# Performance work log

Hardware: AMD Instinct MI355X
Metric: run time of the kernel (lower is better)

## Reference

```python
import jax, jax.numpy as jnp
import numpy as np

NUM_HEADS = 16


def setup_inputs() -> dict:
    key = jax.random.key(0)
    ks = jax.random.split(key, 7)
    B_, N, C = 512, 64, 512
    x = jax.random.normal(ks[0], (B_, N, C), dtype=jnp.float32)
    attn_bias = jax.random.normal(ks[1], (NUM_HEADS, N, N), dtype=jnp.float32)
    mask = jax.random.normal(ks[2], (B_, N, N), dtype=jnp.float32)
    qkv_w = jax.random.normal(ks[3], (3 * C, C), dtype=jnp.float32) * (C ** -0.5)
    qkv_b = jax.random.normal(ks[4], (3 * C,), dtype=jnp.float32) * 0.02
    proj_w = jax.random.normal(ks[5], (C, C), dtype=jnp.float32) * (C ** -0.5)
    proj_b = jax.random.normal(ks[6], (C,), dtype=jnp.float32) * 0.02
    return {"x": x, "attn_bias": attn_bias, "mask": mask,
            "qkv_w": qkv_w, "qkv_b": qkv_b, "proj_w": proj_w, "proj_b": proj_b}


def reference(x, attn_bias, mask, qkv_w, qkv_b, proj_w, proj_b):
    B_, N, C = x.shape
    H = NUM_HEADS
    hd = C // H
    scale = hd ** -0.5
    # qkv projection: (B_, N, 3, H, hd) -> (3, B_, H, N, hd)
    qkv = (x @ qkv_w.T + qkv_b).reshape(B_, N, 3, H, hd)
    qkv = jnp.transpose(qkv, (2, 0, 3, 1, 4))
    q, k, v = qkv[0], qkv[1], qkv[2]
    attn = jnp.einsum('bhnd,bhmd->bhnm', q * scale, k)  # (B_, H, N, N)
    attn = attn + attn_bias            # (H, N, N) broadcasts over batch
    attn = attn + mask[:, None]        # (B_, 1, N, N)
    attn = jax.nn.softmax(attn, axis=-1)
    out = jnp.einsum('bhnm,bhmd->bhnd', attn, v)
    out = jnp.transpose(out, (0, 2, 1, 3)).reshape(B_, N, C)
    return out @ proj_w.T + proj_b
```

## Files before the change

### kernel.cpp

```cpp
#include <hip/hip_runtime.h>
#include <stdint.h>

typedef __attribute__((ext_vector_type(8))) __bf16 bf16x8;
typedef __attribute__((ext_vector_type(4))) float f32x4;
typedef __attribute__((ext_vector_type(4))) float fl4;
typedef __attribute__((ext_vector_type(8))) unsigned short us8;
typedef __attribute__((ext_vector_type(4))) unsigned short us4;

__device__ __forceinline__ unsigned short f2bf(float f) {
  union { float f; unsigned int u; } v;
  v.f = f;
  unsigned int r = v.u + 0x7FFFu + ((v.u >> 16) & 1u);
  return (unsigned short)(r >> 16);
}

#define GLOAD_LDS16(g, l)                                                   \
  __builtin_amdgcn_global_load_lds(                                         \
      (__attribute__((address_space(1))) void*)(g),                         \
      (__attribute__((address_space(3))) void*)(l), 16, 0, 0)

__global__ void f32_to_bf16_kernel(const float* __restrict__ in,
                                   unsigned short* __restrict__ out, int n) {
  int i = (blockIdx.x * blockDim.x + threadIdx.x) * 4;
  if (i + 3 < n) {
    fl4 v = *(const fl4*)(in + i);
    us4 o;
    o[0] = f2bf(v[0]);
    o[1] = f2bf(v[1]);
    o[2] = f2bf(v[2]);
    o[3] = f2bf(v[3]);
    *(us4*)(out + i) = o;
  }
}

template <bool OUT_BF16>
__global__ __launch_bounds__(256, 2) void gemm_nt_kernel(
    const unsigned short* __restrict__ A, const unsigned short* __restrict__ B,
    const float* __restrict__ bias, void* __restrict__ Cout, int M, int N,
    int K) {
  __shared__ __align__(16) unsigned short lA[128 * 64];
  __shared__ __align__(16) unsigned short lB[128 * 64];

  const int tid = threadIdx.x;
  const int lane = tid & 63;
  const int wid = tid >> 6;
  const int wr = (wid >> 1) * 64;
  const int wc = (wid & 1) * 64;
  const int bm = blockIdx.x * 128;
  const int bn = blockIdx.y * 128;

  const f32x4 zero4 = {0.f, 0.f, 0.f, 0.f};
  f32x4 acc[4][4];
#pragma unroll
  for (int m = 0; m < 4; ++m)
#pragma unroll
    for (int n = 0; n < 4; ++n) acc[m][n] = zero4;

  const int srow = tid >> 3;
  const int scol = (tid & 7) << 3;
  unsigned short* Ab = (unsigned short*)(A + (size_t)(bm + srow) * K + scol);
  unsigned short* Bb = (unsigned short*)(B + (size_t)(bn + srow) * K + scol);
  unsigned short* lAb = lA + srow * 64 + scol;
  unsigned short* lBb = lB + srow * 64 + scol;

  const int lr = lane & 15;
  const int lk8 = (lane >> 4) * 8;

  const int nkt = K >> 6;
  for (int kt = 0; kt < nkt; ++kt) {
#pragma unroll
    for (int i = 0; i < 4; ++i) {
      GLOAD_LDS16(Ab + (size_t)(i * 32) * K + kt * 64, lAb + i * 32 * 64);
      GLOAD_LDS16(Bb + (size_t)(i * 32) * K + kt * 64, lBb + i * 32 * 64);
    }
    asm volatile("s_waitcnt vmcnt(0)" ::: "memory");
    __syncthreads();
#pragma unroll
    for (int kk = 0; kk < 2; ++kk) {
      bf16x8 af[4], bfr[4];
#pragma unroll
      for (int m = 0; m < 4; ++m)
        af[m] = *(const bf16x8*)(lA + (wr + m * 16 + lr) * 64 + kk * 32 + lk8);
#pragma unroll
      for (int n = 0; n < 4; ++n)
        bfr[n] = *(const bf16x8*)(lB + (wc + n * 16 + lr) * 64 + kk * 32 + lk8);
#pragma unroll
      for (int m = 0; m < 4; ++m)
#pragma unroll
        for (int n = 0; n < 4; ++n)
          acc[m][n] = __builtin_amdgcn_mfma_f32_16x16x32_bf16(af[m], bfr[n],
                                                              acc[m][n], 0, 0, 0);
    }
    __syncthreads();
  }

  const int crow0 = bm + wr + (lane >> 4) * 4;
  const int ccol0 = bn + wc + lr;
#pragma unroll
  for (int n = 0; n < 4; ++n) {
    const int col = ccol0 + n * 16;
    const float bv = bias[col];
#pragma unroll
    for (int m = 0; m < 4; ++m) {
#pragma unroll
      for (int j = 0; j < 4; ++j) {
        const int row = crow0 + m * 16 + j;
        const float val = acc[m][n][j] + bv;
        if (OUT_BF16)
          ((unsigned short*)Cout)[(size_t)row * N + col] = f2bf(val);
        else
          ((float*)Cout)[(size_t)row * N + col] = val;
      }
    }
  }
}

__global__ __launch_bounds__(256, 2) void attn_kernel(
    const unsigned short* __restrict__ qkv, const float* __restrict__ abias,
    const float* __restrict__ mask, unsigned short* __restrict__ out) {
  __shared__ __align__(16) unsigned short lq[64 * 40];
  __shared__ __align__(16) unsigned short lk[64 * 40];
  __shared__ __align__(16) unsigned short lvT[32 * 72];
  __shared__ __align__(16) float ls[64 * 68];
  __shared__ __align__(16) unsigned short lp[64 * 72];

  const int blk = blockIdx.x;
  const int b = blk >> 4;
  const int h = blk & 15;
  const int tid = threadIdx.x;
  const int lane = tid & 63;
  const int wid = tid >> 6;
  const int lr = lane & 15;
  const int lk8 = (lane >> 4) * 8;

  {
    const int r = tid >> 2;
    const int d0 = (tid & 3) * 8;
    const size_t base = (size_t)(b * 64 + r) * 1536 + h * 32 + d0;
    us8 qv = *(const us8*)(qkv + base);
    us8 kv = *(const us8*)(qkv + base + 512);
    us8 vv = *(const us8*)(qkv + base + 1024);
    *(us8*)(lq + r * 40 + d0) = qv;
    *(us8*)(lk + r * 40 + d0) = kv;
#pragma unroll
    for (int i = 0; i < 8; ++i) lvT[(d0 + i) * 72 + r] = vv[i];
  }
  __syncthreads();

  f32x4 s[4];
  {
    bf16x8 aq = *(const bf16x8*)(lq + (wid * 16 + lr) * 40 + lk8);
#pragma unroll
    for (int n = 0; n < 4; ++n) {
      bf16x8 bk = *(const bf16x8*)(lk + (n * 16 + lr) * 40 + lk8);
      f32x4 z = {0.f, 0.f, 0.f, 0.f};
      s[n] = __builtin_amdgcn_mfma_f32_16x16x32_bf16(aq, bk, z, 0, 0, 0);
    }
  }
  const float scale = 0.17677669529663687f;
  const int sr0 = wid * 16 + (lane >> 4) * 4;
#pragma unroll
  for (int n = 0; n < 4; ++n) {
    const int col = n * 16 + lr;
#pragma unroll
    for (int j = 0; j < 4; ++j) {
      const int row = sr0 + j;
      ls[row * 68 + col] = s[n][j] * scale + abias[(h * 64 + row) * 64 + col] +
                           mask[((size_t)b * 64 + row) * 64 + col];
    }
  }
  __syncthreads();

  {
    const int r = tid >> 2;
    const int c0 = (tid & 3) * 16;
    float e[16];
#pragma unroll
    for (int i = 0; i < 16; ++i) e[i] = ls[r * 68 + c0 + i];
    float mx = e[0];
#pragma unroll
    for (int i = 1; i < 16; ++i) mx = fmaxf(mx, e[i]);
    mx = fmaxf(mx, __shfl_xor(mx, 1));
    mx = fmaxf(mx, __shfl_xor(mx, 2));
    float sum = 0.f;
#pragma unroll
    for (int i = 0; i < 16; ++i) {
      e[i] = __expf(e[i] - mx);
      sum += e[i];
    }
    sum += __shfl_xor(sum, 1);
    sum += __shfl_xor(sum, 2);
    const float inv = 1.f / sum;
#pragma unroll
    for (int i = 0; i < 16; ++i) lp[r * 72 + c0 + i] = f2bf(e[i] * inv);
  }
  __syncthreads();

  f32x4 o[2];
  o[0] = (f32x4){0.f, 0.f, 0.f, 0.f};
  o[1] = o[0];
#pragma unroll
  for (int kk = 0; kk < 2; ++kk) {
    bf16x8 pa = *(const bf16x8*)(lp + (wid * 16 + lr) * 72 + kk * 32 + lk8);
#pragma unroll
    for (int d = 0; d < 2; ++d) {
      bf16x8 vb = *(const bf16x8*)(lvT + (d * 16 + lr) * 72 + kk * 32 + lk8);
      o[d] = __builtin_amdgcn_mfma_f32_16x16x32_bf16(pa, vb, o[d], 0, 0, 0);
    }
  }
#pragma unroll
  for (int d = 0; d < 2; ++d) {
    const int col = h * 32 + d * 16 + lr;
#pragma unroll
    for (int j = 0; j < 4; ++j) {
      const int row = sr0 + j;
      out[(size_t)(b * 64 + row) * 512 + col] = f2bf(o[d][j]);
    }
  }
}

extern "C" void kernel_launch(void* const* d_in, const int* in_sizes, int n_in,
                              void* d_out, int out_size, void* d_ws,
                              size_t ws_size, hipStream_t stream) {
  (void)in_sizes; (void)n_in; (void)out_size; (void)ws_size;
  const float* x = (const float*)d_in[0];
  const float* abias = (const float*)d_in[1];
  const float* mask = (const float*)d_in[2];
  const float* qkv_w = (const float*)d_in[3];
  const float* qkv_b = (const float*)d_in[4];
  const float* proj_w = (const float*)d_in[5];
  const float* proj_b = (const float*)d_in[6];

  char* ws = (char*)d_ws;
  unsigned short* ws_x = (unsigned short*)(ws);
  unsigned short* ws_qkv = (unsigned short*)(ws + 33554432);
  unsigned short* ws_wq = (unsigned short*)(ws + 134217728);
  unsigned short* ws_wp = (unsigned short*)(ws + 135790592);
  unsigned short* ws_att = ws_x;

  f32_to_bf16_kernel<<<16384, 256, 0, stream>>>(x, ws_x, 16777216);
  f32_to_bf16_kernel<<<768, 256, 0, stream>>>(qkv_w, ws_wq, 786432);
  f32_to_bf16_kernel<<<256, 256, 0, stream>>>(proj_w, ws_wp, 262144);

  gemm_nt_kernel<true><<<dim3(256, 12), 256, 0, stream>>>(
      ws_x, ws_wq, qkv_b, ws_qkv, 32768, 1536, 512);

  attn_kernel<<<8192, 256, 0, stream>>>(ws_qkv, abias, mask, ws_att);

  gemm_nt_kernel<false><<<dim3(256, 4), 256, 0, stream>>>(
      ws_att, ws_wp, proj_b, d_out, 32768, 512, 512);
}
```

Measured before the change: 294.2 us.

## Double-buffer GEMM with swizzled LDS, register softmax in attention, remap block order

The GEMM now double-buffers its LDS tiles, so the next K tile's global-to-LDS load overlaps the current MFMAs. It also XOR-swizzles the LDS layout to avoid bank conflicts and uses a 1D grid with grouped tile ordering for better L2 reuse. The attention kernel drops the fp32 score staging in LDS and does the softmax on the MFMA accumulators in registers using cross-lane shuffles. That removes a barrier and LDS traffic, and raises the occupancy hint to 4. The attention block index is also permuted to interleave batches across XCDs.

```diff
diff --git a/kernel.cpp b/kernel.cpp
--- a/kernel.cpp
+++ b/kernel.cpp
@@ -16,7 +16,7 @@
 
 #define GLOAD_LDS16(g, l)                                                   \
   __builtin_amdgcn_global_load_lds(                                         \
-      (__attribute__((address_space(1))) void*)(g),                         \
+      (const __attribute__((address_space(1))) void*)(g),                   \
       (__attribute__((address_space(3))) void*)(l), 16, 0, 0)
 
 __global__ void f32_to_bf16_kernel(const float* __restrict__ in,
@@ -34,67 +34,90 @@
 }
 
 template <bool OUT_BF16>
-__global__ __launch_bounds__(256, 2) void gemm_nt_kernel(
+__global__ __launch_bounds__(256, 2) void gemm128_kernel(
     const unsigned short* __restrict__ A, const unsigned short* __restrict__ B,
     const float* __restrict__ bias, void* __restrict__ Cout, int M, int N,
-    int K) {
-  __shared__ __align__(16) unsigned short lA[128 * 64];
-  __shared__ __align__(16) unsigned short lB[128 * 64];
+    int K, int NT) {
+  __shared__ __align__(16) unsigned short lds[32768];
+  char* base = (char*)lds;
 
   const int tid = threadIdx.x;
   const int lane = tid & 63;
   const int wid = tid >> 6;
+  const int lr = lane & 15;
+  const int lg = lane >> 4;
   const int wr = (wid >> 1) * 64;
   const int wc = (wid & 1) * 64;
-  const int bm = blockIdx.x * 128;
-  const int bn = blockIdx.y * 128;
-
-  const f32x4 zero4 = {0.f, 0.f, 0.f, 0.f};
+
+  const int bid = blockIdx.x;
+  const int bm = ((bid & 31) + (bid / (32 * NT)) * 32) << 7;
+  const int bn = (((bid >> 5) % NT)) << 7;
+
+  const int srow = tid >> 3;
+  const int scolsw = ((tid & 7) << 4) ^ ((srow & 7) << 4);
+  const char* Ag = (const char*)A;
+  const char* Bg = (const char*)B;
+  const size_t Kb = (size_t)K * 2;
+
+#define STAGE(kt, p)                                                          \
+  {                                                                           \
+    char* la_ = base + (p) * 32768;                                           \
+    char* lb_ = la_ + 16384;                                                  \
+    _Pragma("unroll") for (int i_ = 0; i_ < 4; ++i_) {                        \
+      GLOAD_LDS16(Ag + (size_t)(bm + srow + i_ * 32) * Kb + (kt) * 128 + scolsw, \
+                  la_ + srow * 128 + i_ * 4096 + (tid & 7) * 16);             \
+      GLOAD_LDS16(Bg + (size_t)(bn + srow + i_ * 32) * Kb + (kt) * 128 + scolsw, \
+                  lb_ + srow * 128 + i_ * 4096 + (tid & 7) * 16);             \
+    }                                                                         \
+  }
+
+  const int swz = (lr & 7) << 4;
+  const int ck0 = (lg << 4) ^ swz;
+  const int ck1 = (64 + (lg << 4)) ^ swz;
+
   f32x4 acc[4][4];
 #pragma unroll
   for (int m = 0; m < 4; ++m)
 #pragma unroll
-    for (int n = 0; n < 4; ++n) acc[m][n] = zero4;
-
-  const int srow = tid >> 3;
-  const int scol = (tid & 7) << 3;
-  unsigned short* Ab = (unsigned short*)(A + (size_t)(bm + srow) * K + scol);
-  unsigned short* Bb = (unsigned short*)(B + (size_t)(bn + srow) * K + scol);
-  unsigned short* lAb = lA + srow * 64 + scol;
-  unsigned short* lBb = lB + srow * 64 + scol;
-
-  const int lr = lane & 15;
-  const int lk8 = (lane >> 4) * 8;
+    for (int n = 0; n < 4; ++n) acc[m][n] = (f32x4){0.f, 0.f, 0.f, 0.f};
 
   const int nkt = K >> 6;
+
+  STAGE(0, 0);
+  __syncthreads();
+
   for (int kt = 0; kt < nkt; ++kt) {
-#pragma unroll
-    for (int i = 0; i < 4; ++i) {
-      GLOAD_LDS16(Ab + (size_t)(i * 32) * K + kt * 64, lAb + i * 32 * 64);
-      GLOAD_LDS16(Bb + (size_t)(i * 32) * K + kt * 64, lBb + i * 32 * 64);
-    }
-    asm volatile("s_waitcnt vmcnt(0)" ::: "memory");
+    const int p = kt & 1;
+    if (kt + 1 < nkt) STAGE(kt + 1, p ^ 1);
+
+    const char* la = base + p * 32768;
+    const char* lb = la + 16384;
+    bf16x8 af[4][2], bfr[4][2];
+#pragma unroll
+    for (int m = 0; m < 4; ++m) {
+      const int arow = (wr + m * 16 + lr) << 7;
+      af[m][0] = *(const bf16x8*)(la + arow + ck0);
+      af[m][1] = *(const bf16x8*)(la + arow + ck1);
+    }
+#pragma unroll
+    for (int n = 0; n < 4; ++n) {
+      const int brow = (wc + n * 16 + lr) << 7;
+      bfr[n][0] = *(const bf16x8*)(lb + brow + ck0);
+      bfr[n][1] = *(const bf16x8*)(lb + brow + ck1);
+    }
+#pragma unroll
+    for (int kk = 0; kk < 2; ++kk)
+#pragma unroll
+      for (int m = 0; m < 4; ++m)
+#pragma unroll
+        for (int n = 0; n < 4; ++n)
+          acc[m][n] = __builtin_amdgcn_mfma_f32_16x16x32_bf16(
+              af[m][kk], bfr[n][kk], acc[m][n], 0, 0, 0);
     __syncthreads();
-#pragma unroll
-    for (int kk = 0; kk < 2; ++kk) {
-      bf16x8 af[4], bfr[4];
-#pragma unroll
-      for (int m = 0; m < 4; ++m)
-        af[m] = *(const bf16x8*)(lA + (wr + m * 16 + lr) * 64 + kk * 32 + lk8);
-#pragma unroll
-      for (int n = 0; n < 4; ++n)
-        bfr[n] = *(const bf16x8*)(lB + (wc + n * 16 + lr) * 64 + kk * 32 + lk8);
-#pragma unroll
-      for (int m = 0; m < 4; ++m)
-#pragma unroll
-        for (int n = 0; n < 4; ++n)
-          acc[m][n] = __builtin_amdgcn_mfma_f32_16x16x32_bf16(af[m], bfr[n],
-                                                              acc[m][n], 0, 0, 0);
-    }
-    __syncthreads();
-  }
-
-  const int crow0 = bm + wr + (lane >> 4) * 4;
+  }
+#undef STAGE
+
+  const int crow0 = bm + wr + lg * 4;
   const int ccol0 = bn + wc + lr;
 #pragma unroll
   for (int n = 0; n < 4; ++n) {
@@ -115,31 +138,32 @@
   }
 }
 
-__global__ __launch_bounds__(256, 2) void attn_kernel(
+__global__ __launch_bounds__(256, 4) void attn_kernel(
     const unsigned short* __restrict__ qkv, const float* __restrict__ abias,
     const float* __restrict__ mask, unsigned short* __restrict__ out) {
   __shared__ __align__(16) unsigned short lq[64 * 40];
   __shared__ __align__(16) unsigned short lk[64 * 40];
   __shared__ __align__(16) unsigned short lvT[32 * 72];
-  __shared__ __align__(16) float ls[64 * 68];
   __shared__ __align__(16) unsigned short lp[64 * 72];
 
-  const int blk = blockIdx.x;
-  const int b = blk >> 4;
-  const int h = blk & 15;
+  const int bid = blockIdx.x;
+  const int id2 = (bid & 7) * 1024 + (bid >> 3);
+  const int b = id2 >> 4;
+  const int h = id2 & 15;
   const int tid = threadIdx.x;
   const int lane = tid & 63;
   const int wid = tid >> 6;
   const int lr = lane & 15;
-  const int lk8 = (lane >> 4) * 8;
+  const int lg = lane >> 4;
+  const int lk8 = lg * 8;
 
   {
     const int r = tid >> 2;
     const int d0 = (tid & 3) * 8;
-    const size_t base = (size_t)(b * 64 + r) * 1536 + h * 32 + d0;
-    us8 qv = *(const us8*)(qkv + base);
-    us8 kv = *(const us8*)(qkv + base + 512);
-    us8 vv = *(const us8*)(qkv + base + 1024);
+    const size_t bse = (size_t)(b * 64 + r) * 1536 + h * 32 + d0;
+    us8 qv = *(const us8*)(qkv + bse);
+    us8 kv = *(const us8*)(qkv + bse + 512);
+    us8 vv = *(const us8*)(qkv + bse + 1024);
     *(us8*)(lq + r * 40 + d0) = qv;
     *(us8*)(lk + r * 40 + d0) = kv;
 #pragma unroll
@@ -158,42 +182,46 @@
     }
   }
   const float scale = 0.17677669529663687f;
-  const int sr0 = wid * 16 + (lane >> 4) * 4;
-#pragma unroll
-  for (int n = 0; n < 4; ++n) {
-    const int col = n * 16 + lr;
+  const int row0 = wid * 16 + lg * 4;
+#pragma unroll
+  for (int j = 0; j < 4; ++j) {
+    const int row = row0 + j;
+    const float* ab = abias + (h * 64 + row) * 64 + lr;
+    const float* mk = mask + ((size_t)b * 64 + row) * 64 + lr;
+#pragma unroll
+    for (int n = 0; n < 4; ++n)
+      s[n][j] = s[n][j] * scale + ab[n * 16] + mk[n * 16];
+  }
+
+  float mx[4], sm[4];
+#pragma unroll
+  for (int j = 0; j < 4; ++j)
+    mx[j] = fmaxf(fmaxf(s[0][j], s[1][j]), fmaxf(s[2][j], s[3][j]));
+#pragma unroll
+  for (int xm = 1; xm <= 8; xm <<= 1)
+#pragma unroll
+    for (int j = 0; j < 4; ++j) mx[j] = fmaxf(mx[j], __shfl_xor(mx[j], xm));
+#pragma unroll
+  for (int j = 0; j < 4; ++j) sm[j] = 0.f;
+#pragma unroll
+  for (int n = 0; n < 4; ++n)
 #pragma unroll
     for (int j = 0; j < 4; ++j) {
-      const int row = sr0 + j;
-      ls[row * 68 + col] = s[n][j] * scale + abias[(h * 64 + row) * 64 + col] +
-                           mask[((size_t)b * 64 + row) * 64 + col];
-    }
-  }
-  __syncthreads();
-
-  {
-    const int r = tid >> 2;
-    const int c0 = (tid & 3) * 16;
-    float e[16];
-#pragma unroll
-    for (int i = 0; i < 16; ++i) e[i] = ls[r * 68 + c0 + i];
-    float mx = e[0];
-#pragma unroll
-    for (int i = 1; i < 16; ++i) mx = fmaxf(mx, e[i]);
-    mx = fmaxf(mx, __shfl_xor(mx, 1));
-    mx = fmaxf(mx, __shfl_xor(mx, 2));
-    float sum = 0.f;
-#pragma unroll
-    for (int i = 0; i < 16; ++i) {
-      e[i] = __expf(e[i] - mx);
-      sum += e[i];
-    }
-    sum += __shfl_xor(sum, 1);
-    sum += __shfl_xor(sum, 2);
-    const float inv = 1.f / sum;
-#pragma unroll
-    for (int i = 0; i < 16; ++i) lp[r * 72 + c0 + i] = f2bf(e[i] * inv);
-  }
+      const float e = __expf(s[n][j] - mx[j]);
+      s[n][j] = e;
+      sm[j] += e;
+    }
+#pragma unroll
+  for (int xm = 1; xm <= 8; xm <<= 1)
+#pragma unroll
+    for (int j = 0; j < 4; ++j) sm[j] += __shfl_xor(sm[j], xm);
+#pragma unroll
+  for (int j = 0; j < 4; ++j) sm[j] = 1.f / sm[j];
+#pragma unroll
+  for (int n = 0; n < 4; ++n)
+#pragma unroll
+    for (int j = 0; j < 4; ++j)
+      lp[(row0 + j) * 72 + n * 16 + lr] = f2bf(s[n][j] * sm[j]);
   __syncthreads();
 
   f32x4 o[2];
@@ -213,7 +241,7 @@
     const int col = h * 32 + d * 16 + lr;
 #pragma unroll
     for (int j = 0; j < 4; ++j) {
-      const int row = sr0 + j;
+      const int row = row0 + j;
       out[(size_t)(b * 64 + row) * 512 + col] = f2bf(o[d][j]);
     }
   }
@@ -242,11 +270,11 @@
   f32_to_bf16_kernel<<<768, 256, 0, stream>>>(qkv_w, ws_wq, 786432);
   f32_to_bf16_kernel<<<256, 256, 0, stream>>>(proj_w, ws_wp, 262144);
 
-  gemm_nt_kernel<true><<<dim3(256, 12), 256, 0, stream>>>(
-      ws_x, ws_wq, qkv_b, ws_qkv, 32768, 1536, 512);
+  gemm128_kernel<true><<<3072, 256, 0, stream>>>(ws_x, ws_wq, qkv_b, ws_qkv,
+                                                 32768, 1536, 512, 12);
 
   attn_kernel<<<8192, 256, 0, stream>>>(ws_qkv, abias, mask, ws_att);
 
-  gemm_nt_kernel<false><<<dim3(256, 4), 256, 0, stream>>>(
-      ws_att, ws_wp, proj_b, d_out, 32768, 512, 512);
-}
+  gemm128_kernel<false><<<1024, 256, 0, stream>>>(ws_att, ws_wp, proj_b, d_out,
+                                                  32768, 512, 512, 4);
+}
```

New measurement: 266.6 us. -9.4%, faster.
